# Optimization experiments

Hardware: AMD Instinct MI355X
Metric: run time of the kernel (lower is better)

Reference implementation:

```python
import jax, jax.numpy as jnp
import numpy as np

B, L, H, HEADS = 32, 512, 1024, 16
LN_EPS = 1e-5
NEG_INF = -1e9


def _layernorm(x, g, b):
    m = jnp.mean(x, axis=-1, keepdims=True)
    v = jnp.mean(jnp.square(x - m), axis=-1, keepdims=True)
    return (x - m) * jax.lax.rsqrt(v + LN_EPS) * g + b


def setup_inputs() -> dict:
    key = jax.random.key(0)
    ks = jax.random.split(key, 10)
    # deterministic variable graph sizes -> padding mask with fixed total valid count
    lengths = L - (np.arange(B) % 16) * 8          # per-graph node counts
    mask_np = np.arange(L)[None, :] < lengths[:, None]   # [B, L] bool
    node_idx = np.nonzero(mask_np.reshape(-1))[0].astype(np.int32)  # [14464]
    s = 0.02
    inp = {
        "x_dense": jax.random.normal(ks[0], (B, L, H), jnp.float32),
        "batch_CLS": jax.random.normal(ks[1], (B, 1, H), jnp.float32),
        "mask": jnp.asarray(mask_np),
        "node_idx": jnp.asarray(node_idx),
        "WQ": jax.random.normal(ks[2], (H, H), jnp.float32) * s,
        "bQ": jnp.zeros((H,), jnp.float32),
        "WK": jax.random.normal(ks[3], (H, H), jnp.float32) * s,
        "bK": jnp.zeros((H,), jnp.float32),
        "WV": jax.random.normal(ks[4], (H, H), jnp.float32) * s,
        "bV": jnp.zeros((H,), jnp.float32),
        "WO": jax.random.normal(ks[5], (H, H), jnp.float32) * s,
        "bO": jnp.zeros((H,), jnp.float32),
        "g1": jnp.ones((H,), jnp.float32),
        "beta1": jnp.zeros((H,), jnp.float32),
        "Wf1": jax.random.normal(ks[6], (H, 2 * H), jnp.float32) * s,
        "bf1": jnp.zeros((2 * H,), jnp.float32),
        "Wf2": jax.random.normal(ks[7], (2 * H, H), jnp.float32) * s,
        "bf2": jnp.zeros((H,), jnp.float32),
        "g2": jnp.ones((H,), jnp.float32),
        "beta2": jnp.zeros((H,), jnp.float32),
    }
    return inp


def reference(x_dense, batch_CLS, mask, node_idx, WQ, bQ, WK, bK, WV, bV,
              WO, bO, g1, beta1, Wf1, bf1, Wf2, bf2, g2, beta2):
    b, l, h = x_dense.shape
    d = h // HEADS
    # append CLS token; attention mask gets an always-True CLS column
    xd = jnp.concatenate([x_dense, batch_CLS], axis=1)            # [B, S, H], S = L+1
    am = jnp.concatenate([mask, jnp.ones((b, 1), bool)], axis=1)  # [B, S]
    S = l + 1
    Qh = (xd @ WQ + bQ).reshape(b, S, HEADS, d)
    Kh = (xd @ WK + bK).reshape(b, S, HEADS, d)
    Vh = (xd @ WV + bV).reshape(b, S, HEADS, d)
    scores = jnp.einsum('bqhd,bkhd->bhqk', Qh, Kh) / jnp.sqrt(jnp.float32(d))
    # additive padding mask over keys (masked_attention=True, clustering=False)
    scores = scores + jnp.where(am, 0.0, NEG_INF)[:, None, None, :]
    A = jax.nn.softmax(scores, axis=-1)                           # [B, h, S, S]
    # torch layout: A_torch[hh*B + b] == A[b, hh] -> cls_attn [h*B, S]
    cls_attn = jax.lax.stop_gradient(
        jnp.transpose(A[:, :, -1, :], (1, 0, 2)).reshape(HEADS * b, S))
    ctx = jnp.einsum('bhqk,bkhd->bqhd', A, Vh).reshape(b, S, h)
    attn_out = ctx @ WO + bO + xd                                  # residual
    cls_rows = attn_out[:, -1, :]                                  # [B, H]
    nodes = attn_out[:, :-1, :].reshape(b * l, h)[node_idx]        # valid nodes packed
    packed = jnp.concatenate([nodes, cls_rows], axis=0)            # [Ntot+B, H]
    h1 = _layernorm(packed, g1, beta1)
    ffn = jax.nn.relu(h1 @ Wf1 + bf1) @ Wf2 + bf2
    out = _layernorm(ffn + h1, g2, beta2)
    return out, cls_attn
```

## Files before the change

kernel.cpp:

```cpp
#include <hip/hip_runtime.h>
#include <stdint.h>

typedef unsigned short ushort_t;
typedef __bf16 bf16x8 __attribute__((ext_vector_type(8)));
typedef float  f32x4  __attribute__((ext_vector_type(4)));
typedef unsigned short ushortx8 __attribute__((ext_vector_type(8)));

constexpr int CB  = 32;
constexpr int CL  = 512;
constexpr int CNH = 16;
constexpr int CDH = 64;
constexpr int CS  = 513;
constexpr int CNR = CB * CS;
constexpr int CVTS = 576;
constexpr int CST = 136;

__device__ __forceinline__ float bf2f(ushort_t u) {
  return __builtin_bit_cast(float, (uint32_t)u << 16);
}
__device__ __forceinline__ ushort_t f2bf(float f) {
  uint32_t x = __builtin_bit_cast(uint32_t, f);
  x += 0x7fffu + ((x >> 16) & 1u);
  return (ushort_t)(x >> 16);
}

typedef __attribute__((address_space(1))) const unsigned int GU32;
typedef __attribute__((address_space(3))) unsigned int LU32;
__device__ __forceinline__ void gld16(const void* g, void* l) {
  __builtin_amdgcn_global_load_lds((GU32*)g, (LU32*)l, 16, 0, 0);
}

__global__ __launch_bounds__(256)
void k_prep(const float* __restrict__ WQ, const float* __restrict__ WK,
            const float* __restrict__ WV, const float* __restrict__ WO,
            const float* __restrict__ Wf1, const float* __restrict__ Wf2,
            ushort_t* __restrict__ Wqkvt, ushort_t* __restrict__ Wot,
            ushort_t* __restrict__ Wf1t, ushort_t* __restrict__ Wf2t,
            const float* __restrict__ bQ, const float* __restrict__ bK,
            const float* __restrict__ bV, float* __restrict__ bqkv,
            int* __restrict__ lens, int* __restrict__ starts,
            const int* __restrict__ node_idx, int nn,
            const float* __restrict__ xd, const float* __restrict__ cls,
            ushort_t* __restrict__ XDP) {
  const int bid = blockIdx.x;
  const int t = threadIdx.x;
  if (bid == 8192) {
    for (int i = t; i < 3072; i += 256)
      bqkv[i] = (i < 1024) ? bQ[i] : (i < 2048 ? bK[i - 1024] : bV[i - 2048]);
    if (t < CB) {
      int bounds[2];
#pragma unroll
      for (int e = 0; e < 2; ++e) {
        int target = (t + e) << 9;
        int lo = 0, hi = nn;
        while (lo < hi) {
          int mid = (lo + hi) >> 1;
          if (node_idx[mid] < target) lo = mid + 1; else hi = mid;
        }
        bounds[e] = lo;
      }
      starts[t] = bounds[0];
      lens[t] = bounds[1] - bounds[0];
    }
    return;
  }
  if (bid > 8192) {
    size_t e = ((size_t)(bid - 8193) * 256 + t) * 8;
    int p = (int)(e >> 10);
    int col = (int)(e & 1023);
    const float* src = (p < nn) ? (xd + ((size_t)node_idx[p] << 10) + col)
                                : (cls + ((size_t)(p - nn) << 10) + col);
    float4 v0 = ((const float4*)src)[0];
    float4 v1 = ((const float4*)src)[1];
    ushortx8 o;
    o[0] = f2bf(v0.x); o[1] = f2bf(v0.y); o[2] = f2bf(v0.z); o[3] = f2bf(v0.w);
    o[4] = f2bf(v1.x); o[5] = f2bf(v1.y); o[6] = f2bf(v1.z); o[7] = f2bf(v1.w);
    *((ushortx8*)(XDP + e)) = o;
    return;
  }
  const float* in; ushort_t* out; int R, C, tx32, ty32;
  if (bid < 3072) {
    int which = bid >> 10, tt = bid & 1023;
    in = (which == 0) ? WQ : (which == 1 ? WK : WV);
    out = Wqkvt + (size_t)which * 1024 * 1024;
    R = 1024; C = 1024; tx32 = tt & 31; ty32 = tt >> 5;
  } else if (bid < 4096) {
    int tt = bid - 3072;
    in = WO; out = Wot; R = 1024; C = 1024; tx32 = tt & 31; ty32 = tt >> 5;
  } else if (bid < 6144) {
    int tt = bid - 4096;
    in = Wf1; out = Wf1t; R = 1024; C = 2048; tx32 = tt & 63; ty32 = tt >> 6;
  } else {
    int tt = bid - 6144;
    in = Wf2; out = Wf2t; R = 2048; C = 1024; tx32 = tt & 31; ty32 = tt >> 5;
  }
  __shared__ float tle[32][33];
  const int c0 = tx32 * 32, r0 = ty32 * 32;
  const int tx = t & 31, ty = t >> 5;
#pragma unroll
  for (int i = 0; i < 4; ++i) {
    int r = ty + i * 8;
    tle[r][tx] = in[(size_t)(r0 + r) * C + c0 + tx];
  }
  __syncthreads();
#pragma unroll
  for (int i = 0; i < 4; ++i) {
    int r = ty + i * 8;
    out[(size_t)(c0 + r) * R + r0 + tx] = f2bf(tle[tx][r]);
  }
}

template <int EPI>
__global__ __launch_bounds__(256, 2)
void k_gemm(const ushort_t* __restrict__ A, const ushort_t* __restrict__ Bt,
            int M, int N, int K,
            const float* __restrict__ pb,
            const ushort_t* __restrict__ pauxB,
            const int* __restrict__ nidx, int nn,
            ushort_t* __restrict__ outB0, ushort_t* __restrict__ outB1) {
  __shared__ __align__(16) ushort_t sh[128 * CST];
  ushort_t* As = sh;
  ushort_t* Bs = sh + 8192;
  const int tid = threadIdx.x;
  const int lane = tid & 63, wid = tid >> 6;
  const int wr = wid >> 1, wc = wid & 1;
  const int lm = lane & 15, lq = lane >> 4;
  const int m0 = blockIdx.y * 128, n0 = blockIdx.x * 128;

  f32x4 acc[4][4];
  const f32x4 z4 = {0.f, 0.f, 0.f, 0.f};
#pragma unroll
  for (int i = 0; i < 4; ++i)
#pragma unroll
    for (int j = 0; j < 4; ++j) acc[i][j] = z4;

  for (int kt = 0; kt < K; kt += 64) {
    __syncthreads();
#pragma unroll
    for (int it = 0; it < 4; ++it) {
      int c = it * 256 + tid;
      int r = c >> 3, jc = c & 7;
      int j = jc ^ (r & 7);
      int ra = m0 + r; if (ra > M - 1) ra = M - 1;
      gld16(A + (size_t)ra * K + kt + j * 8, As + (size_t)c * 8);
    }
#pragma unroll
    for (int it = 0; it < 4; ++it) {
      int c = it * 256 + tid;
      int r = c >> 3, jc = c & 7;
      int j = jc ^ (r & 7);
      gld16(Bt + (size_t)(n0 + r) * K + kt + j * 8, Bs + (size_t)c * 8);
    }
    __syncthreads();
#pragma unroll
    for (int kk = 0; kk < 2; ++kk) {
      bf16x8 af[4], bfr[4];
#pragma unroll
      for (int mi = 0; mi < 4; ++mi) {
        int R = wr * 64 + mi * 16 + lm;
        int u = R * 8 + ((kk * 4 + lq) ^ (R & 7));
        af[mi] = *reinterpret_cast<const bf16x8*>(As + u * 8);
      }
#pragma unroll
      for (int ni = 0; ni < 4; ++ni) {
        int R = wc * 64 + ni * 16 + lm;
        int u = R * 8 + ((kk * 4 + lq) ^ (R & 7));
        bfr[ni] = *reinterpret_cast<const bf16x8*>(Bs + u * 8);
      }
#pragma unroll
      for (int mi = 0; mi < 4; ++mi)
#pragma unroll
        for (int ni = 0; ni < 4; ++ni)
          acc[mi][ni] = __builtin_amdgcn_mfma_f32_16x16x32_bf16(af[mi], bfr[ni], acc[mi][ni], 0, 0, 0);
    }
  }

  __syncthreads();
  ushort_t* Cs = sh;
#pragma unroll
  for (int mi = 0; mi < 4; ++mi) {
#pragma unroll
    for (int ni = 0; ni < 4; ++ni) {
#pragma unroll
      for (int j = 0; j < 4; ++j) {
        int row = wr * 64 + mi * 16 + lq * 4 + j;
        int c128 = wc * 64 + ni * 16 + lm;
        int r = m0 + row;
        int rc = r < M ? r : M - 1;
        int c = n0 + c128;
        float v = acc[mi][ni][j] + pb[c];
        if constexpr (EPI == 1) v += bf2f(pauxB[(size_t)rc * 1024 + c]);
        else if constexpr (EPI == 2) v = v > 0.f ? v : 0.f;
        Cs[row * CST + c128] = f2bf(v);
      }
    }
  }
  __syncthreads();

  if (EPI == 0 && n0 >= 2048) {
    const int row = tid & 127;
    const int half = tid >> 7;
    const int r = m0 + row;
    if (r < M) {
      int b, s;
      if (r < nn) { int idx = nidx[r]; b = idx >> 9; s = idx & 511; }
      else        { b = r - nn; s = 512; }
      const int cvbase = n0 - 2048;
#pragma unroll 8
      for (int ci = 0; ci < 64; ++ci) {
        int c128 = half * 64 + ci;
        int cv = cvbase + c128;
        int h = cv >> 6, d = cv & 63;
        outB1[((size_t)(b * CNH + h) * CDH + d) * CVTS + s] = Cs[row * CST + c128];
      }
    }
  } else {
    const int ld = (EPI == 1) ? 1024 : 2048;
#pragma unroll
    for (int it = 0; it < 8; ++it) {
      int g = it * 256 + tid;
      int row = g >> 4, c16 = g & 15;
      int r = m0 + row;
      if (r >= M) continue;
      ushortx8 val = *reinterpret_cast<const ushortx8*>(&Cs[row * CST + c16 * 8]);
      *reinterpret_cast<ushortx8*>(&outB0[(size_t)r * ld + n0 + c16 * 8]) = val;
    }
  }
}

__global__ __launch_bounds__(256, 2)
void k_attn(const ushort_t* __restrict__ QK, const ushort_t* __restrict__ Vt,
            const int* __restrict__ lens, const int* __restrict__ starts, int nn,
            ushort_t* __restrict__ CTX) {
  __shared__ __align__(16) ushort_t Ks[64 * 64];
  __shared__ __align__(16) ushort_t Vs[64 * 64];
  __shared__ __align__(16) ushort_t Ps[4][16][72];

  const int tid = threadIdx.x;
  const int lane = tid & 63, wid = tid >> 6;
  const int lm = lane & 15, lq = lane >> 4;

  const int bidx = blockIdx.x;
  const int qt = bidx >> 9;
  const int hb = bidx & 511;
  const int h = hb & 15, b = hb >> 4;
  const int len = lens[b];
  if (qt * 128 >= len) return;
  const int st0 = starts[b];
  const int clsrow = nn + b;

  const int qbase = qt * 128 + wid * 16;

  bf16x8 aq[2][2];
#pragma unroll
  for (int t2 = 0; t2 < 2; ++t2) {
    int qr = qbase + t2 * 64 + lm; if (qr > len - 1) qr = len - 1;
    const ushort_t* qptr = QK + (size_t)(st0 + qr) * 2048 + h * CDH + lq * 8;
    aq[t2][0] = *reinterpret_cast<const bf16x8*>(qptr);
    aq[t2][1] = *reinterpret_cast<const bf16x8*>(qptr + 32);
  }

  const f32x4 z4 = {0.f, 0.f, 0.f, 0.f};
  f32x4 acc[2][4];
#pragma unroll
  for (int t2 = 0; t2 < 2; ++t2)
#pragma unroll
    for (int i = 0; i < 4; ++i) acc[t2][i] = z4;
  float lrow[2][4] = {{0.f, 0.f, 0.f, 0.f}, {0.f, 0.f, 0.f, 0.f}};

  const size_t vtBase = (size_t)(b * CNH + h) * CDH * CVTS;

  for (int kc = 0; kc < 9; ++kc) {
    const int k0 = kc * 64;
    if (k0 >= len && kc != 8) continue;
    __syncthreads();
#pragma unroll
    for (int it = 0; it < 2; ++it) {
      int c = it * 256 + tid;
      int r = c >> 3, jc = c & 7;
      int j = jc ^ (r & 7);
      int k = k0 + r;
      int krow = (k < len) ? (st0 + k) : clsrow;
      gld16(QK + (size_t)krow * 2048 + 1024 + h * CDH + j * 8, Ks + (size_t)c * 8);
    }
#pragma unroll
    for (int it = 0; it < 2; ++it) {
      int c = it * 256 + tid;
      int r = c >> 3, jc = c & 7;
      int j = jc ^ (r & 7);
      gld16(Vt + vtBase + (size_t)r * CVTS + k0 + j * 8, Vs + (size_t)c * 8);
    }
    __syncthreads();

#pragma unroll
    for (int t2 = 0; t2 < 2; ++t2) {
      f32x4 sc[4];
#pragma unroll
      for (int st = 0; st < 4; ++st) sc[st] = z4;
#pragma unroll
      for (int kk = 0; kk < 2; ++kk) {
        bf16x8 kb[4];
#pragma unroll
        for (int st = 0; st < 4; ++st) {
          int R = st * 16 + lm;
          int u = R * 8 + ((kk * 4 + lq) ^ (R & 7));
          kb[st] = *reinterpret_cast<const bf16x8*>(Ks + u * 8);
        }
#pragma unroll
        for (int st = 0; st < 4; ++st)
          sc[st] = __builtin_amdgcn_mfma_f32_16x16x32_bf16(aq[t2][kk], kb[st], sc[st], 0, 0, 0);
      }

      float p[4][4];
      float sum[4] = {0.f, 0.f, 0.f, 0.f};
#pragma unroll
      for (int st = 0; st < 4; ++st) {
        int kg = k0 + st * 16 + lm;
        float madd = ((kg < len) || (kg == 512)) ? 0.f : -1e9f;
#pragma unroll
        for (int r2 = 0; r2 < 4; ++r2) {
          float e = __expf(sc[st][r2] * 0.125f + madd);
          p[st][r2] = e;
          sum[r2] += e;
        }
      }
#pragma unroll
      for (int r2 = 0; r2 < 4; ++r2) {
        sum[r2] += __shfl_xor(sum[r2], 1);
        sum[r2] += __shfl_xor(sum[r2], 2);
        sum[r2] += __shfl_xor(sum[r2], 4);
        sum[r2] += __shfl_xor(sum[r2], 8);
        lrow[t2][r2] += sum[r2];
      }
#pragma unroll
      for (int st = 0; st < 4; ++st)
#pragma unroll
        for (int r2 = 0; r2 < 4; ++r2)
          Ps[wid][lq * 4 + r2][st * 16 + lm] = f2bf(p[st][r2]);

      bf16x8 ap[2];
      ap[0] = *reinterpret_cast<const bf16x8*>(&Ps[wid][lm][lq * 8]);
      ap[1] = *reinterpret_cast<const bf16x8*>(&Ps[wid][lm][32 + lq * 8]);
#pragma unroll
      for (int kk = 0; kk < 2; ++kk) {
#pragma unroll
        for (int dt = 0; dt < 4; ++dt) {
          int R = dt * 16 + lm;
          int u = R * 8 + ((kk * 4 + lq) ^ (R & 7));
          bf16x8 vb = *reinterpret_cast<const bf16x8*>(Vs + u * 8);
          acc[t2][dt] = __builtin_amdgcn_mfma_f32_16x16x32_bf16(ap[kk], vb, acc[t2][dt], 0, 0, 0);
        }
      }
    }
  }

#pragma unroll
  for (int t2 = 0; t2 < 2; ++t2) {
    float inv[4];
#pragma unroll
    for (int r2 = 0; r2 < 4; ++r2) inv[r2] = 1.f / lrow[t2][r2];
#pragma unroll
    for (int dt = 0; dt < 4; ++dt) {
#pragma unroll
      for (int r2 = 0; r2 < 4; ++r2) {
        int q = qbase + t2 * 64 + lq * 4 + r2;
        if (q < len)
          CTX[(size_t)(st0 + q) * 1024 + h * CDH + dt * 16 + lm] = f2bf(acc[t2][dt][r2] * inv[r2]);
      }
    }
  }
}

__global__ __launch_bounds__(64)
void k_attn_cls(const ushort_t* __restrict__ QK, const ushort_t* __restrict__ Vt,
                const int* __restrict__ lens, const int* __restrict__ starts, int nn,
                ushort_t* __restrict__ CTX, float* __restrict__ clsOut) {
  const int bid = blockIdx.x;
  const int h = bid >> 5, b = bid & 31;
  const int l = threadIdx.x;
  __shared__ float qv[64];
  __shared__ float probs[516];
  const int st0 = starts[b];
  const int clsrow = nn + b;
  qv[l] = bf2f(QK[(size_t)clsrow * 2048 + h * CDH + l]);
  __syncthreads();
  const int len = lens[b];

  float sc[9];
  float mx = -INFINITY;
#pragma unroll
  for (int i = 0; i < 9; ++i) {
    int k = l + 64 * i;
    if (k < CS) {
      int krow = (k < len) ? (st0 + k) : clsrow;
      const ushort_t* kr = QK + (size_t)krow * 2048 + 1024 + h * CDH;
      float a2 = 0.f;
#pragma unroll
      for (int d0 = 0; d0 < 64; d0 += 8) {
        bf16x8 kv = *reinterpret_cast<const bf16x8*>(kr + d0);
#pragma unroll
        for (int j = 0; j < 8; ++j) a2 += qv[d0 + j] * (float)kv[j];
      }
      a2 *= 0.125f;
      if (!((k < len) || (k == 512))) a2 += -1e9f;
      sc[i] = a2;
      mx = fmaxf(mx, a2);
    } else {
      sc[i] = -INFINITY;
    }
  }
  for (int m2 = 1; m2 < 64; m2 <<= 1) mx = fmaxf(mx, __shfl_xor(mx, m2));
  float sum = 0.f, p[9];
#pragma unroll
  for (int i = 0; i < 9; ++i) { p[i] = __expf(sc[i] - mx); sum += p[i]; }
  for (int m2 = 1; m2 < 64; m2 <<= 1) sum += __shfl_xor(sum, m2);
  float invs = 1.f / sum;
#pragma unroll
  for (int i = 0; i < 9; ++i) {
    int k = l + 64 * i;
    if (k < CS) {
      float pr = p[i] * invs;
      clsOut[(size_t)bid * CS + k] = pr;
      probs[k] = pr;
    }
  }
  __syncthreads();
  const ushort_t* vr = Vt + ((size_t)(b * CNH + h) * CDH + l) * CVTS;
  float a2 = 0.f;
  for (int k = 0; k < 512; k += 8) {
    bf16x8 vv = *reinterpret_cast<const bf16x8*>(vr + k);
#pragma unroll
    for (int j = 0; j < 8; ++j) a2 += probs[k + j] * (float)vv[j];
  }
  a2 += probs[512] * bf2f(vr[512]);
  CTX[(size_t)clsrow * 1024 + h * CDH + l] = f2bf(a2);
}

template <int MODE>
__global__ __launch_bounds__(256)
void k_ln(const ushort_t* __restrict__ X,
          const float* __restrict__ g, const float* __restrict__ be,
          float* __restrict__ outF, ushort_t* __restrict__ outB) {
  const int p = blockIdx.x;
  const int t = threadIdx.x;
  const uint2 u = ((const uint2*)(X + (size_t)p * 1024))[t];
  float v0 = bf2f((ushort_t)(u.x & 0xffff)), v1 = bf2f((ushort_t)(u.x >> 16));
  float v2 = bf2f((ushort_t)(u.y & 0xffff)), v3 = bf2f((ushort_t)(u.y >> 16));
  float s1 = v0 + v1 + v2 + v3;
  float s2 = v0 * v0 + v1 * v1 + v2 * v2 + v3 * v3;
  for (int m2 = 1; m2 < 64; m2 <<= 1) {
    s1 += __shfl_xor(s1, m2);
    s2 += __shfl_xor(s2, m2);
  }
  __shared__ float red[8];
  const int lane = t & 63, wid = t >> 6;
  if (lane == 0) { red[wid] = s1; red[4 + wid] = s2; }
  __syncthreads();
  s1 = red[0] + red[1] + red[2] + red[3];
  s2 = red[4] + red[5] + red[6] + red[7];
  float mean = s1 * (1.f / 1024.f);
  float var = s2 * (1.f / 1024.f) - mean * mean;
  float rs = rsqrtf(var + 1e-5f);
  float4 gv = ((const float4*)g)[t];
  float4 bv = ((const float4*)be)[t];
  float y0 = (v0 - mean) * rs * gv.x + bv.x;
  float y1 = (v1 - mean) * rs * gv.y + bv.y;
  float y2 = (v2 - mean) * rs * gv.z + bv.z;
  float y3 = (v3 - mean) * rs * gv.w + bv.w;
  if constexpr (MODE == 0) {
    uint2 o;
    o.x = (unsigned)f2bf(y0) | ((unsigned)f2bf(y1) << 16);
    o.y = (unsigned)f2bf(y2) | ((unsigned)f2bf(y3) << 16);
    ((uint2*)(outB + (size_t)p * 1024))[t] = o;
  } else {
    ((float4*)(outF + (size_t)p * 1024))[t] = make_float4(y0, y1, y2, y3);
  }
}

extern "C" void kernel_launch(void* const* d_in, const int* in_sizes, int n_in,
                              void* d_out, int out_size, void* d_ws, size_t ws_size,
                              hipStream_t stream) {
  const float* x_dense = (const float*)d_in[0];
  const float* bcls    = (const float*)d_in[1];
  const int*   node_idx = (const int*)d_in[3];
  const float* WQ = (const float*)d_in[4];
  const float* bQ = (const float*)d_in[5];
  const float* WK = (const float*)d_in[6];
  const float* bK = (const float*)d_in[7];
  const float* WV = (const float*)d_in[8];
  const float* bV = (const float*)d_in[9];
  const float* WO = (const float*)d_in[10];
  const float* bO = (const float*)d_in[11];
  const float* g1 = (const float*)d_in[12];
  const float* be1 = (const float*)d_in[13];
  const float* Wf1 = (const float*)d_in[14];
  const float* bf1 = (const float*)d_in[15];
  const float* Wf2 = (const float*)d_in[16];
  const float* bf2 = (const float*)d_in[17];
  const float* g2 = (const float*)d_in[18];
  const float* be2 = (const float*)d_in[19];

  const int nn = in_sizes[3];
  const int NP = nn + CB;

  char* ws = (char*)d_ws;
  const size_t oWqkv = 0;
  const size_t oWo   = oWqkv + (size_t)3072 * 1024 * 2;
  const size_t oWf1  = oWo + (size_t)1024 * 1024 * 2;
  const size_t oWf2  = oWf1 + (size_t)2048 * 1024 * 2;
  const size_t oBqkv = oWf2 + (size_t)1024 * 2048 * 2;
  const size_t oLens = oBqkv + 3072 * 4;
  const size_t oRA = (oLens + 512 + 255) & ~(size_t)255;
  const size_t szRA = (size_t)CNR * 2048 * 2;
  const size_t oRB = oRA + szRA;
  const size_t szRB = (size_t)CNR * 1024 * 2;
  const size_t oRC = oRB + szRB;
  const size_t szVt = (size_t)CB * CNH * CDH * CVTS * 2;
  const size_t oRD = oRC + szVt;

  ushort_t* Wqkvt = (ushort_t*)(ws + oWqkv);
  ushort_t* Wot   = (ushort_t*)(ws + oWo);
  ushort_t* Wf1t  = (ushort_t*)(ws + oWf1);
  ushort_t* Wf2t  = (ushort_t*)(ws + oWf2);
  float* bqkv = (float*)(ws + oBqkv);
  int* lens   = (int*)(ws + oLens);
  int* starts = lens + CB;
  ushort_t* QK  = (ushort_t*)(ws + oRA);
  ushort_t* CTX = (ushort_t*)(ws + oRB);
  ushort_t* Vt  = (ushort_t*)(ws + oRC);
  ushort_t* XDP = (ushort_t*)(ws + oRD);
  ushort_t* AO  = (ushort_t*)(ws + oRA);
  ushort_t* H1B = (ushort_t*)(ws + oRB);
  ushort_t* G   = (ushort_t*)(ws + oRA);
  ushort_t* F   = (ushort_t*)(ws + oRC);

  float* out0 = (float*)d_out;
  float* clsOut = out0 + (size_t)NP * 1024;

  dim3 blk(256);
  hipMemsetAsync(Vt, 0, szVt, stream);

  const int nPack = NP / 2;
  k_prep<<<dim3(8193 + nPack), blk, 0, stream>>>(
      WQ, WK, WV, WO, Wf1, Wf2, Wqkvt, Wot, Wf1t, Wf2t,
      bQ, bK, bV, bqkv, lens, starts, node_idx, nn, x_dense, bcls, XDP);

  const int mtP = (NP + 127) / 128;
  k_gemm<0><<<dim3(3072 / 128, mtP), blk, 0, stream>>>(
      XDP, Wqkvt, NP, 3072, 1024, bqkv, nullptr, node_idx, nn, QK, Vt);
  k_attn<<<dim3(CB * CNH * 4), blk, 0, stream>>>(QK, Vt, lens, starts, nn, CTX);
  k_attn_cls<<<dim3(CB * CNH), dim3(64), 0, stream>>>(QK, Vt, lens, starts, nn, CTX, clsOut);
  k_gemm<1><<<dim3(1024 / 128, mtP), blk, 0, stream>>>(
      CTX, Wot, NP, 1024, 1024, bO, XDP, nullptr, nn, AO, nullptr);
  k_ln<0><<<dim3(NP), blk, 0, stream>>>(AO, g1, be1, nullptr, H1B);
  k_gemm<2><<<dim3(2048 / 128, mtP), blk, 0, stream>>>(
      H1B, Wf1t, NP, 2048, 1024, bf1, nullptr, nullptr, nn, G, nullptr);
  k_gemm<1><<<dim3(1024 / 128, mtP), blk, 0, stream>>>(
      G, Wf2t, NP, 1024, 2048, bf2, H1B, nullptr, nn, F, nullptr);
  k_ln<1><<<dim3(NP), blk, 0, stream>>>(F, g2, be2, out0, nullptr);
  (void)ws_size; (void)out_size; (void)n_in;
}
```

Before: 466.6 us.

## Keep attention probabilities in registers via transposed score MFMA and bpermute

Swaps the MFMA operand order so each lane holds scores for one query across several keys. The softmax row sum then becomes a per-lane accumulation, reduced only once at the end. Probabilities are packed to bf16 with v_cvt_pk_bf16_f32 and redistributed with ds_bpermute, replacing the per-wave LDS scratch buffer and its store/load round trip. The scale is folded into exp2, and the early-exit check for empty query tiles is removed. The exchange costs extra bpermute traffic and some added index arithmetic in the epilogue.

New measurement: 481.4 us. 1.03x slower.

```diff
diff --git a/kernel.cpp b/kernel.cpp
--- a/kernel.cpp
+++ b/kernel.cpp
@@ -5,6 +5,7 @@
 typedef __bf16 bf16x8 __attribute__((ext_vector_type(8)));
 typedef float  f32x4  __attribute__((ext_vector_type(4)));
 typedef unsigned short ushortx8 __attribute__((ext_vector_type(8)));
+typedef unsigned int u32x4 __attribute__((ext_vector_type(4)));
 
 constexpr int CB  = 32;
 constexpr int CL  = 512;
@@ -22,6 +23,11 @@
   uint32_t x = __builtin_bit_cast(uint32_t, f);
   x += 0x7fffu + ((x >> 16) & 1u);
   return (ushort_t)(x >> 16);
+}
+__device__ __forceinline__ uint32_t cvtpk_bf16(float lo, float hi) {
+  uint32_t r;
+  asm volatile("v_cvt_pk_bf16_f32 %0, %1, %2" : "=v"(r) : "v"(lo), "v"(hi));
+  return r;
 }
 
 typedef __attribute__((address_space(1))) const unsigned int GU32;
@@ -234,7 +240,6 @@
             ushort_t* __restrict__ CTX) {
   __shared__ __align__(16) ushort_t Ks[64 * 64];
   __shared__ __align__(16) ushort_t Vs[64 * 64];
-  __shared__ __align__(16) ushort_t Ps[4][16][72];
 
   const int tid = threadIdx.x;
   const int lane = tid & 63, wid = tid >> 6;
@@ -245,7 +250,6 @@
   const int hb = bidx & 511;
   const int h = hb & 15, b = hb >> 4;
   const int len = lens[b];
-  if (qt * 128 >= len) return;
   const int st0 = starts[b];
   const int clsrow = nn + b;
 
@@ -266,9 +270,10 @@
   for (int t2 = 0; t2 < 2; ++t2)
 #pragma unroll
     for (int i = 0; i < 4; ++i) acc[t2][i] = z4;
-  float lrow[2][4] = {{0.f, 0.f, 0.f, 0.f}, {0.f, 0.f, 0.f, 0.f}};
+  float lrow[2] = {0.f, 0.f};
 
   const size_t vtBase = (size_t)(b * CNH + h) * CDH * CVTS;
+  const float C1 = 0.125f * 1.44269504f;
 
   for (int kc = 0; kc < 9; ++kc) {
     const int k0 = kc * 64;
@@ -308,47 +313,44 @@
         }
 #pragma unroll
         for (int st = 0; st < 4; ++st)
-          sc[st] = __builtin_amdgcn_mfma_f32_16x16x32_bf16(aq[t2][kk], kb[st], sc[st], 0, 0, 0);
-      }
-
-      float p[4][4];
-      float sum[4] = {0.f, 0.f, 0.f, 0.f};
+          sc[st] = __builtin_amdgcn_mfma_f32_16x16x32_bf16(kb[st], aq[t2][kk], sc[st], 0, 0, 0);
+      }
+
+      uint32_t ulo[4], uhi[4];
+      float lsum = 0.f;
 #pragma unroll
       for (int st = 0; st < 4; ++st) {
-        int kg = k0 + st * 16 + lm;
-        float madd = ((kg < len) || (kg == 512)) ? 0.f : -1e9f;
+        float pr[4];
 #pragma unroll
         for (int r2 = 0; r2 < 4; ++r2) {
-          float e = __expf(sc[st][r2] * 0.125f + madd);
-          p[st][r2] = e;
-          sum[r2] += e;
+          int kg = k0 + st * 16 + lq * 4 + r2;
+          float madd = ((kg < len) || (kg == 512)) ? 0.f : -1e9f;
+          float e = exp2f(sc[st][r2] * C1 + madd);
+          pr[r2] = e;
+          lsum += e;
         }
-      }
-#pragma unroll
-      for (int r2 = 0; r2 < 4; ++r2) {
-        sum[r2] += __shfl_xor(sum[r2], 1);
-        sum[r2] += __shfl_xor(sum[r2], 2);
-        sum[r2] += __shfl_xor(sum[r2], 4);
-        sum[r2] += __shfl_xor(sum[r2], 8);
-        lrow[t2][r2] += sum[r2];
-      }
-#pragma unroll
-      for (int st = 0; st < 4; ++st)
-#pragma unroll
-        for (int r2 = 0; r2 < 4; ++r2)
-          Ps[wid][lq * 4 + r2][st * 16 + lm] = f2bf(p[st][r2]);
-
-      bf16x8 ap[2];
-      ap[0] = *reinterpret_cast<const bf16x8*>(&Ps[wid][lm][lq * 8]);
-      ap[1] = *reinterpret_cast<const bf16x8*>(&Ps[wid][lm][32 + lq * 8]);
+        ulo[st] = cvtpk_bf16(pr[0], pr[1]);
+        uhi[st] = cvtpk_bf16(pr[2], pr[3]);
+      }
+      lrow[t2] += lsum;
+
 #pragma unroll
       for (int kk = 0; kk < 2; ++kk) {
+        uint32_t lo_s = (lq & 2) ? ulo[kk * 2 + 1] : ulo[kk * 2];
+        uint32_t hi_s = (lq & 2) ? uhi[kk * 2 + 1] : uhi[kk * 2];
+        int srcA = (lm + ((lq & 1) << 5)) << 2;
+        u32x4 w;
+        w[0] = (uint32_t)__builtin_amdgcn_ds_bpermute(srcA,      (int)lo_s);
+        w[1] = (uint32_t)__builtin_amdgcn_ds_bpermute(srcA,      (int)hi_s);
+        w[2] = (uint32_t)__builtin_amdgcn_ds_bpermute(srcA + 64, (int)lo_s);
+        w[3] = (uint32_t)__builtin_amdgcn_ds_bpermute(srcA + 64, (int)hi_s);
+        bf16x8 ap = __builtin_bit_cast(bf16x8, w);
 #pragma unroll
         for (int dt = 0; dt < 4; ++dt) {
           int R = dt * 16 + lm;
           int u = R * 8 + ((kk * 4 + lq) ^ (R & 7));
           bf16x8 vb = *reinterpret_cast<const bf16x8*>(Vs + u * 8);
-          acc[t2][dt] = __builtin_amdgcn_mfma_f32_16x16x32_bf16(ap[kk], vb, acc[t2][dt], 0, 0, 0);
+          acc[t2][dt] = __builtin_amdgcn_mfma_f32_16x16x32_bf16(ap, vb, acc[t2][dt], 0, 0, 0);
         }
       }
     }
@@ -356,16 +358,20 @@
 
 #pragma unroll
   for (int t2 = 0; t2 < 2; ++t2) {
-    float inv[4];
-#pragma unroll
-    for (int r2 = 0; r2 < 4; ++r2) inv[r2] = 1.f / lrow[t2][r2];
-#pragma unroll
-    for (int dt = 0; dt < 4; ++dt) {
-#pragma unroll
-      for (int r2 = 0; r2 < 4; ++r2) {
-        int q = qbase + t2 * 64 + lq * 4 + r2;
-        if (q < len)
-          CTX[(size_t)(st0 + q) * 1024 + h * CDH + dt * 16 + lm] = f2bf(acc[t2][dt][r2] * inv[r2]);
+    float s0 = lrow[t2];
+    s0 += __shfl_xor(s0, 16);
+    s0 += __shfl_xor(s0, 32);
+    float inv = 1.f / s0;
+    uint32_t invb = __builtin_bit_cast(uint32_t, inv);
+#pragma unroll
+    for (int r2 = 0; r2 < 4; ++r2) {
+      uint32_t ib = (uint32_t)__builtin_amdgcn_ds_bpermute((lq * 4 + r2) << 2, (int)invb);
+      float invq = __builtin_bit_cast(float, ib);
+      int q = qbase + t2 * 64 + lq * 4 + r2;
+      if (q < len) {
+#pragma unroll
+        for (int dt = 0; dt < 4; ++dt)
+          CTX[(size_t)(st0 + q) * 1024 + h * CDH + dt * 16 + lm] = f2bf(acc[t2][dt][r2] * invq);
       }
     }
   }
```
